# Kernel tuning notes

Hardware: AMD Instinct MI355X
Metric: run time of the kernel (lower is better)

The kernel has to match this reference:

```python
import jax, jax.numpy as jnp
import numpy as np

T, IN_DIM, H1, H2 = 64, 84, 128, 84
BATCH = 8192


def _glorot(key, shape, fan):
    bound = 1.0 / np.sqrt(fan)
    return jax.random.uniform(key, shape, jnp.float32, -bound, bound)


def setup_inputs() -> dict:
    key = jax.random.key(0)
    ks = jax.random.split(key, 13)
    x = jax.random.normal(ks[0], (BATCH, T, IN_DIM, 1), jnp.float32)
    # rnn1 layer 0: 84 -> 128
    w_ih_l0 = _glorot(ks[1], (H1, IN_DIM), H1)
    w_hh_l0 = _glorot(ks[2], (H1, H1), H1)
    b_ih_l0 = _glorot(ks[3], (H1,), H1)
    b_hh_l0 = _glorot(ks[4], (H1,), H1)
    # rnn1 layer 1: 128 -> 128
    w_ih_l1 = _glorot(ks[5], (H1, H1), H1)
    w_hh_l1 = _glorot(ks[6], (H1, H1), H1)
    b_ih_l1 = _glorot(ks[7], (H1,), H1)
    b_hh_l1 = _glorot(ks[8], (H1,), H1)
    # rnn2: 128 -> 84
    w_ih_l2 = _glorot(ks[9], (H2, H1), H2)
    w_hh_l2 = _glorot(ks[10], (H2, H2), H2)
    b_ih_l2 = _glorot(ks[11], (H2,), H2)
    b_hh_l2 = _glorot(ks[12], (H2,), H2)
    return {
        "x": x,
        "w_ih_l0": w_ih_l0, "w_hh_l0": w_hh_l0, "b_ih_l0": b_ih_l0, "b_hh_l0": b_hh_l0,
        "w_ih_l1": w_ih_l1, "w_hh_l1": w_hh_l1, "b_ih_l1": b_ih_l1, "b_hh_l1": b_hh_l1,
        "w_ih_l2": w_ih_l2, "w_hh_l2": w_hh_l2, "b_ih_l2": b_ih_l2, "b_hh_l2": b_hh_l2,
    }


def _elman_layer(x, w_ih, w_hh, b_ih, b_hh):
    # x: (B, T, I) -> (B, T, H); h_t = tanh(x_t W_ih^T + b_ih + h_{t-1} W_hh^T + b_hh)
    # Precompute the input projection for all timesteps as one big GEMM.
    xp = jnp.einsum('bti,hi->bth', x, w_ih) + (b_ih + b_hh)  # (B, T, H)
    h0 = jnp.zeros((x.shape[0], w_hh.shape[0]), x.dtype)

    def step(h, xp_t):
        h = jnp.tanh(xp_t + h @ w_hh.T)
        return h, h

    _, ys = jax.lax.scan(step, h0, jnp.swapaxes(xp, 0, 1))  # (T, B, H)
    return jnp.swapaxes(ys, 0, 1)


def reference(x,
              w_ih_l0, w_hh_l0, b_ih_l0, b_hh_l0,
              w_ih_l1, w_hh_l1, b_ih_l1, b_hh_l1,
              w_ih_l2, w_hh_l2, b_ih_l2, b_hh_l2):
    x_ = jnp.squeeze(x, -1)                                   # (B, 64, 84)
    h = _elman_layer(x_, w_ih_l0, w_hh_l0, b_ih_l0, b_hh_l0)  # (B, 64, 128)
    h = _elman_layer(h, w_ih_l1, w_hh_l1, b_ih_l1, b_hh_l1)   # (B, 64, 128)
    h = _elman_layer(h, w_ih_l2, w_hh_l2, b_ih_l2, b_hh_l2)   # (B, 64, 84)
    return h[..., None]                                       # (B, 64, 84, 1)
```

## Files before the change

kernel.cpp:

```cpp
#include <hip/hip_runtime.h>


typedef __bf16 bf16x8 __attribute__((ext_vector_type(8)));
typedef float  f32x4  __attribute__((ext_vector_type(4)));
typedef float  f32x16 __attribute__((ext_vector_type(16)));
typedef unsigned short u16;
typedef unsigned int   u32;
typedef u16 u16x8 __attribute__((ext_vector_type(8)));
typedef u16 u16x4 __attribute__((ext_vector_type(4)));

#define MFMA32(a, b, c) __builtin_amdgcn_mfma_f32_32x32x16_bf16((a), (b), (c), 0, 0, 0)

__device__ __forceinline__ float bf2f(u16 v) {
    return __builtin_bit_cast(float, (u32)v << 16);
}
__device__ __forceinline__ u16 f2bf(float f) {
    u32 u = __builtin_bit_cast(u32, f);
    u = u + 0x7fffu + ((u >> 16) & 1u);
    return (u16)(u >> 16);
}
__device__ __forceinline__ float tanh_fast(float x) {
    float xc = fminf(fmaxf(x, -12.f), 12.f);
    float e  = __expf(2.f * xc);
    return (e - 1.f) * __builtin_amdgcn_rcpf(e + 1.f);
}
__device__ __forceinline__ bf16x8 ld_lds8(const u16* p) {
    return __builtin_bit_cast(bf16x8, *(const u16x8*)p);
}
__device__ __forceinline__ int aswz(int row, int off) {
    return row * 128 + (off ^ ((row & 7) << 3));
}
__device__ __forceinline__ int xswz(int m, int n) {
    return m * 128 + (n ^ ((m & 7) << 2));
}
__device__ __forceinline__ void store4_hl(u16* ph, u16* pl, f32x4 v) {
    u16x4 hi, lo;
#pragma unroll
    for (int j = 0; j < 4; j++) {
        u16 h = f2bf(v[j]);
        hi[j] = h;
        lo[j] = f2bf(v[j] - bf2f(h));
    }
    *(u16x4*)ph = hi;
    *(u16x4*)pl = lo;
}

struct fragp { bf16x8 h, l; };

__device__ __forceinline__ fragp load_wfrag_hl(const float* W, int Hr, int Kr,
                                               int n, int kbase) {
    u16x8 uh = {0,0,0,0,0,0,0,0}, ul = {0,0,0,0,0,0,0,0};
    if (n < Hr) {
#pragma unroll
        for (int j = 0; j < 8; j++) {
            int k = kbase + j;
            if (k < Kr) {
                float w = W[n * Kr + k];
                u16 hi = f2bf(w);
                uh[j] = hi;
                ul[j] = f2bf(w - bf2f(hi));
            }
        }
    }
    fragp r;
    r.h = __builtin_bit_cast(bf16x8, uh);
    r.l = __builtin_bit_cast(bf16x8, ul);
    return r;
}

__device__ __forceinline__ f32x16 mm3t(const fragp& w, bf16x8 ah, bf16x8 al, f32x16 c) {
    c = MFMA32(w.h, ah, c);
    c = MFMA32(w.l, ah, c);
    c = MFMA32(w.h, al, c);
    return c;
}

__global__ __launch_bounds__(512, 2)
void rnn_fused(const float* __restrict__ x,
               const float* __restrict__ wih0, const float* __restrict__ whh0,
               const float* __restrict__ bih0, const float* __restrict__ bhh0,
               const float* __restrict__ wih1, const float* __restrict__ whh1,
               const float* __restrict__ bih1, const float* __restrict__ bhh1,
               const float* __restrict__ wih2, const float* __restrict__ whh2,
               const float* __restrict__ bih2, const float* __restrict__ bhh2,
               float* __restrict__ out)
{
    __shared__ __align__(16) u16 h0h[2][4096], h0l[2][4096];
    __shared__ __align__(16) u16 h1h[2][4096], h1l[2][4096];
    __shared__ __align__(16) u16 h2h[2][4096], h2l[2][4096];
    __shared__ __align__(16) u16 xbh[2][32][96], xbl[2][32][96];
    __shared__ __align__(16) float xpF[2][4096];
    __shared__ float biasF[3][128];

    const int tid  = threadIdx.x;
    const int wv   = tid >> 6;
    const int lane = tid & 63;
    const int mrow = lane & 31;
    const int q2   = lane >> 5;
    const int kq   = q2 * 8;
    const int q4   = q2 * 4;
    const int aw   = wv & 3;
    const bool isA = (wv < 4);
    const int nb   = aw * 32;
    const int b0   = blockIdx.x * 32;
    const float* xg = x + (long)b0 * 5376;

    { u16* z = &h0h[1][0]; for (int i = tid; i < 4096; i += 512) z[i] = 0; }
    { u16* z = &h0l[1][0]; for (int i = tid; i < 4096; i += 512) z[i] = 0; }
    { u16* z = &h1h[0][0]; for (int i = tid; i < 4096; i += 512) z[i] = 0; }
    { u16* z = &h1l[0][0]; for (int i = tid; i < 4096; i += 512) z[i] = 0; }
    { u16* z = &h2h[1][0]; for (int i = tid; i < 4096; i += 512) z[i] = 0; }
    { u16* z = &h2l[1][0]; for (int i = tid; i < 4096; i += 512) z[i] = 0; }
    for (int i = tid; i < 32 * 12 * 2; i += 512) {
        int par = i / (32 * 12), rem = i - par * 32 * 12;
        int row = rem / 12, col = 84 + rem - row * 12;
        xbh[par][row][col] = 0; xbl[par][row][col] = 0;
    }
    for (int i = tid; i < 32 * 84; i += 512) {
        int row = i / 84, col = i - row * 84;
        float v = xg[(long)row * 5376 + col];
        u16 hi = f2bf(v);
        xbh[0][row][col] = hi;
        xbl[0][row][col] = f2bf(v - bf2f(hi));
    }
    for (int i = tid; i < 384; i += 512) {
        int l = i >> 7, n = i & 127;
        float v = 0.f;
        if (l == 0)      v = bih0[n] + bhh0[n];
        else if (l == 1) v = bih1[n] + bhh1[n];
        else if (n < 84) v = bih2[n] + bhh2[n];
        biasF[l][n] = v;
    }

    __syncthreads();

    if (isA) {
        fragp fhh0[8], fih2[8], fhh2[6];
#pragma unroll
        for (int c = 0; c < 8; c++) {
            fhh0[c] = load_wfrag_hl(whh0, 128, 128, nb + mrow, c * 16 + kq);
            fih2[c] = load_wfrag_hl(wih2,  84, 128, nb + mrow, c * 16 + kq);
        }
#pragma unroll
        for (int c = 0; c < 6; c++)
            fhh2[c] = load_wfrag_hl(whh2, 84, 84, nb + mrow, c * 16 + kq);

        float xs[6];
        for (int rr = 0; rr < 67; ++rr) {
            const int P = rr & 1, PN = P ^ 1;

            if (rr <= 62) {
#pragma unroll
                for (int j = 0; j < 6; j++) {
                    int i = tid + j * 512;
                    if (i < 2688) {
                        int row = i / 84, cc = i - row * 84;
                        xs[j] = xg[(long)row * 5376 + (rr + 1) * 84 + cc];
                    }
                }
            }

            if (rr >= 1 && rr <= 64) {
                f32x16 acc;
#pragma unroll
                for (int g = 0; g < 4; g++) {
                    f32x4 v = *(const f32x4*)&xpF[P][xswz(mrow, nb + g * 8 + q4)];
                    acc[4*g+0] = v[0]; acc[4*g+1] = v[1];
                    acc[4*g+2] = v[2]; acc[4*g+3] = v[3];
                }
                __builtin_amdgcn_s_setprio(1);
#pragma unroll
                for (int c = 0; c < 8; c++) {
                    const int idx = aswz(mrow, c * 16 + kq);
                    acc = mm3t(fhh0[c], ld_lds8(&h0h[P][idx]), ld_lds8(&h0l[P][idx]), acc);
                }
                __builtin_amdgcn_s_setprio(0);
#pragma unroll
                for (int g = 0; g < 4; g++) {
                    const int col = nb + g * 8 + q4;
                    f32x4 v;
                    v[0] = tanh_fast(acc[4*g+0]); v[1] = tanh_fast(acc[4*g+1]);
                    v[2] = tanh_fast(acc[4*g+2]); v[3] = tanh_fast(acc[4*g+3]);
                    const int idx = mrow * 128 + (col ^ ((mrow & 7) << 3));
                    store4_hl(&h0h[PN][idx], &h0l[PN][idx], v);
                }
            }

            if (aw != 3 && rr >= 3) {
                const int t2 = rr - 3;
                f32x16 acc;
#pragma unroll
                for (int g = 0; g < 4; g++) {
                    f32x4 v = *(const f32x4*)&biasF[2][nb + g * 8 + q4];
                    acc[4*g+0] = v[0]; acc[4*g+1] = v[1];
                    acc[4*g+2] = v[2]; acc[4*g+3] = v[3];
                }
                __builtin_amdgcn_s_setprio(1);
#pragma unroll
                for (int c = 0; c < 8; c++) {
                    const int idx = aswz(mrow, c * 16 + kq);
                    acc = mm3t(fih2[c], ld_lds8(&h1h[P][idx]), ld_lds8(&h1l[P][idx]), acc);
                }
#pragma unroll
                for (int c = 0; c < 6; c++) {
                    const int idx = aswz(mrow, c * 16 + kq);
                    acc = mm3t(fhh2[c], ld_lds8(&h2h[P][idx]), ld_lds8(&h2l[P][idx]), acc);
                }
                __builtin_amdgcn_s_setprio(0);
#pragma unroll
                for (int g = 0; g < 4; g++) {
                    const int col = nb + g * 8 + q4;
                    f32x4 v;
                    v[0] = tanh_fast(acc[4*g+0]); v[1] = tanh_fast(acc[4*g+1]);
                    v[2] = tanh_fast(acc[4*g+2]); v[3] = tanh_fast(acc[4*g+3]);
                    const int idx = mrow * 128 + (col ^ ((mrow & 7) << 3));
                    store4_hl(&h2h[PN][idx], &h2l[PN][idx], v);
                    if (col < 84)
                        *(f32x4*)(out + (long)(b0 + mrow) * 5376 + t2 * 84 + col) = v;
                }
            }

            if (rr <= 62) {
#pragma unroll
                for (int j = 0; j < 6; j++) {
                    int i = tid + j * 512;
                    if (i < 2688) {
                        int row = i / 84, cc = i - row * 84;
                        u16 hi = f2bf(xs[j]);
                        xbh[PN][row][cc] = hi;
                        xbl[PN][row][cc] = f2bf(xs[j] - bf2f(hi));
                    }
                }
            }
            __syncthreads();
        }
    } else {
        fragp fih0[6], fih1[8], fhh1[8];
#pragma unroll
        for (int c = 0; c < 6; c++)
            fih0[c] = load_wfrag_hl(wih0, 128, 84, nb + mrow, c * 16 + kq);
#pragma unroll
        for (int c = 0; c < 8; c++) {
            fih1[c] = load_wfrag_hl(wih1, 128, 128, nb + mrow, c * 16 + kq);
            fhh1[c] = load_wfrag_hl(whh1, 128, 128, nb + mrow, c * 16 + kq);
        }

        float xs[6];
        for (int rr = 0; rr < 67; ++rr) {
            const int P = rr & 1, PN = P ^ 1;

            if (rr <= 62) {
#pragma unroll
                for (int j = 0; j < 6; j++) {
                    int i = tid + j * 512;
                    if (i < 2688) {
                        int row = i / 84, cc = i - row * 84;
                        xs[j] = xg[(long)row * 5376 + (rr + 1) * 84 + cc];
                    }
                }
            }

            if (rr >= 2 && rr <= 65) {
                f32x16 acc;
#pragma unroll
                for (int g = 0; g < 4; g++) {
                    f32x4 v = *(const f32x4*)&biasF[1][nb + g * 8 + q4];
                    acc[4*g+0] = v[0]; acc[4*g+1] = v[1];
                    acc[4*g+2] = v[2]; acc[4*g+3] = v[3];
                }
                __builtin_amdgcn_s_setprio(1);
#pragma unroll
                for (int c = 0; c < 8; c++) {
                    const int idx = aswz(mrow, c * 16 + kq);
                    acc = mm3t(fih1[c], ld_lds8(&h0h[P][idx]), ld_lds8(&h0l[P][idx]), acc);
                }
#pragma unroll
                for (int c = 0; c < 8; c++) {
                    const int idx = aswz(mrow, c * 16 + kq);
                    acc = mm3t(fhh1[c], ld_lds8(&h1h[P][idx]), ld_lds8(&h1l[P][idx]), acc);
                }
                __builtin_amdgcn_s_setprio(0);
#pragma unroll
                for (int g = 0; g < 4; g++) {
                    const int col = nb + g * 8 + q4;
                    f32x4 v;
                    v[0] = tanh_fast(acc[4*g+0]); v[1] = tanh_fast(acc[4*g+1]);
                    v[2] = tanh_fast(acc[4*g+2]); v[3] = tanh_fast(acc[4*g+3]);
                    const int idx = mrow * 128 + (col ^ ((mrow & 7) << 3));
                    store4_hl(&h1h[PN][idx], &h1l[PN][idx], v);
                }
            }

            if (rr <= 63) {
                f32x16 acc;
#pragma unroll
                for (int g = 0; g < 4; g++) {
                    f32x4 v = *(const f32x4*)&biasF[0][nb + g * 8 + q4];
                    acc[4*g+0] = v[0]; acc[4*g+1] = v[1];
                    acc[4*g+2] = v[2]; acc[4*g+3] = v[3];
                }
                __builtin_amdgcn_s_setprio(1);
#pragma unroll
                for (int c = 0; c < 6; c++) {
                    const int off = c * 16 + kq;
                    bf16x8 ah = ld_lds8(&xbh[P][mrow][off]);
                    bf16x8 al = ld_lds8(&xbl[P][mrow][off]);
                    acc = mm3t(fih0[c], ah, al, acc);
                }
                __builtin_amdgcn_s_setprio(0);
#pragma unroll
                for (int g = 0; g < 4; g++) {
                    const int n = nb + g * 8 + q4;
                    f32x4 v;
                    v[0] = acc[4*g+0]; v[1] = acc[4*g+1];
                    v[2] = acc[4*g+2]; v[3] = acc[4*g+3];
                    *(f32x4*)&xpF[PN][xswz(mrow, n)] = v;
                }
            }

            if (rr <= 62) {
#pragma unroll
                for (int j = 0; j < 6; j++) {
                    int i = tid + j * 512;
                    if (i < 2688) {
                        int row = i / 84, cc = i - row * 84;
                        u16 hi = f2bf(xs[j]);
                        xbh[PN][row][cc] = hi;
                        xbl[PN][row][cc] = f2bf(xs[j] - bf2f(hi));
                    }
                }
            }
            __syncthreads();
        }
    }
}

extern "C" void kernel_launch(void* const* d_in, const int* in_sizes, int n_in,
                              void* d_out, int out_size, void* d_ws, size_t ws_size,
                              hipStream_t stream) {
    (void)in_sizes; (void)n_in; (void)out_size; (void)d_ws; (void)ws_size;
    const float* x    = (const float*)d_in[0];
    const float* wih0 = (const float*)d_in[1];
    const float* whh0 = (const float*)d_in[2];
    const float* bih0 = (const float*)d_in[3];
    const float* bhh0 = (const float*)d_in[4];
    const float* wih1 = (const float*)d_in[5];
    const float* whh1 = (const float*)d_in[6];
    const float* bih1 = (const float*)d_in[7];
    const float* bhh1 = (const float*)d_in[8];
    const float* wih2 = (const float*)d_in[9];
    const float* whh2 = (const float*)d_in[10];
    const float* bih2 = (const float*)d_in[11];
    const float* bhh2 = (const float*)d_in[12];
    float* out = (float*)d_out;

    rnn_fused<<<dim3(8192 / 32), dim3(512), 0, stream>>>(
        x, wih0, whh0, bih0, bhh0, wih1, whh1, bih1, bhh1,
        wih2, whh2, bih2, bhh2, out);
}
```

Measured before the change: 558.5 us.

## Split fused RNN into per-layer wave groups across 12 waves

```diff
diff --git a/kernel.cpp b/kernel.cpp
--- a/kernel.cpp
+++ b/kernel.cpp
@@ -29,9 +29,6 @@
 }
 __device__ __forceinline__ int aswz(int row, int off) {
     return row * 128 + (off ^ ((row & 7) << 3));
-}
-__device__ __forceinline__ int xswz(int m, int n) {
-    return m * 128 + (n ^ ((m & 7) << 2));
 }
 __device__ __forceinline__ void store4_hl(u16* ph, u16* pl, f32x4 v) {
     u16x4 hi, lo;
@@ -75,7 +72,31 @@
     return c;
 }
 
-__global__ __launch_bounds__(512, 2)
+#define STG_ISSUE(trr)                                                   \
+    {                                                                    \
+        const int tofs = (trr) * 84;                                     \
+        _Pragma("unroll")                                                \
+        for (int j = 0; j < 5; j++) xs[j] = xg[goff[j] + tofs];          \
+        if (tid_s < 128) xs[5] = xg[goff[5] + tofs];                     \
+    }
+#define STG_WRITE(PNv)                                                   \
+    {                                                                    \
+        u16* bh = (&xbh[0][0][0]) + (PNv) * 3072;                        \
+        u16* bl = (&xbl[0][0][0]) + (PNv) * 3072;                        \
+        _Pragma("unroll")                                                \
+        for (int j = 0; j < 5; j++) {                                    \
+            u16 hi = f2bf(xs[j]);                                        \
+            bh[lofs[j]] = hi;                                            \
+            bl[lofs[j]] = f2bf(xs[j] - bf2f(hi));                        \
+        }                                                                \
+        if (tid_s < 128) {                                               \
+            u16 hi = f2bf(xs[5]);                                        \
+            bh[lofs[5]] = hi;                                            \
+            bl[lofs[5]] = f2bf(xs[5] - bf2f(hi));                        \
+        }                                                                \
+    }
+
+__global__ __launch_bounds__(768, 3)
 void rnn_fused(const float* __restrict__ x,
                const float* __restrict__ wih0, const float* __restrict__ whh0,
                const float* __restrict__ bih0, const float* __restrict__ bhh0,
@@ -89,7 +110,6 @@
     __shared__ __align__(16) u16 h1h[2][4096], h1l[2][4096];
     __shared__ __align__(16) u16 h2h[2][4096], h2l[2][4096];
     __shared__ __align__(16) u16 xbh[2][32][96], xbl[2][32][96];
-    __shared__ __align__(16) float xpF[2][4096];
     __shared__ float biasF[3][128];
 
     const int tid  = threadIdx.x;
@@ -99,31 +119,28 @@
     const int q2   = lane >> 5;
     const int kq   = q2 * 8;
     const int q4   = q2 * 4;
-    const int aw   = wv & 3;
-    const bool isA = (wv < 4);
-    const int nb   = aw * 32;
     const int b0   = blockIdx.x * 32;
     const float* xg = x + (long)b0 * 5376;
 
-    { u16* z = &h0h[1][0]; for (int i = tid; i < 4096; i += 512) z[i] = 0; }
-    { u16* z = &h0l[1][0]; for (int i = tid; i < 4096; i += 512) z[i] = 0; }
-    { u16* z = &h1h[0][0]; for (int i = tid; i < 4096; i += 512) z[i] = 0; }
-    { u16* z = &h1l[0][0]; for (int i = tid; i < 4096; i += 512) z[i] = 0; }
-    { u16* z = &h2h[1][0]; for (int i = tid; i < 4096; i += 512) z[i] = 0; }
-    { u16* z = &h2l[1][0]; for (int i = tid; i < 4096; i += 512) z[i] = 0; }
-    for (int i = tid; i < 32 * 12 * 2; i += 512) {
+    { u16* z = &h0h[0][0]; for (int i = tid; i < 4096; i += 768) z[i] = 0; }
+    { u16* z = &h0l[0][0]; for (int i = tid; i < 4096; i += 768) z[i] = 0; }
+    { u16* z = &h1h[1][0]; for (int i = tid; i < 4096; i += 768) z[i] = 0; }
+    { u16* z = &h1l[1][0]; for (int i = tid; i < 4096; i += 768) z[i] = 0; }
+    { u16* z = &h2h[0][0]; for (int i = tid; i < 4096; i += 768) z[i] = 0; }
+    { u16* z = &h2l[0][0]; for (int i = tid; i < 4096; i += 768) z[i] = 0; }
+    for (int i = tid; i < 32 * 12 * 2; i += 768) {
         int par = i / (32 * 12), rem = i - par * 32 * 12;
         int row = rem / 12, col = 84 + rem - row * 12;
         xbh[par][row][col] = 0; xbl[par][row][col] = 0;
     }
-    for (int i = tid; i < 32 * 84; i += 512) {
+    for (int i = tid; i < 2688; i += 768) {
         int row = i / 84, col = i - row * 84;
         float v = xg[(long)row * 5376 + col];
         u16 hi = f2bf(v);
         xbh[0][row][col] = hi;
         xbl[0][row][col] = f2bf(v - bf2f(hi));
     }
-    for (int i = tid; i < 384; i += 512) {
+    for (int i = tid; i < 384; i += 768) {
         int l = i >> 7, n = i & 127;
         float v = 0.f;
         if (l == 0)      v = bih0[n] + bhh0[n];
@@ -131,44 +148,44 @@
         else if (n < 84) v = bih2[n] + bhh2[n];
         biasF[l][n] = v;
     }
-
     __syncthreads();
 
-    if (isA) {
-        fragp fhh0[8], fih2[8], fhh2[6];
-#pragma unroll
-        for (int c = 0; c < 8; c++) {
+    if (wv < 4) {
+        const int nb = wv * 32;
+        fragp fih0[6], fhh0[8];
+#pragma unroll
+        for (int c = 0; c < 6; c++)
+            fih0[c] = load_wfrag_hl(wih0, 128, 84, nb + mrow, c * 16 + kq);
+#pragma unroll
+        for (int c = 0; c < 8; c++)
             fhh0[c] = load_wfrag_hl(whh0, 128, 128, nb + mrow, c * 16 + kq);
-            fih2[c] = load_wfrag_hl(wih2,  84, 128, nb + mrow, c * 16 + kq);
-        }
-#pragma unroll
-        for (int c = 0; c < 6; c++)
-            fhh2[c] = load_wfrag_hl(whh2, 84, 84, nb + mrow, c * 16 + kq);
-
+        const int tid_s = wv * 64 + lane;
+        int goff[6], lofs[6];
+#pragma unroll
+        for (int j = 0; j < 6; j++) {
+            int i = tid_s + j * 512, row = i / 84, cc = i - row * 84;
+            goff[j] = row * 5376 + cc; lofs[j] = row * 96 + cc;
+        }
         float xs[6];
-        for (int rr = 0; rr < 67; ++rr) {
+
+        for (int rr = 0; rr < 66; ++rr) {
             const int P = rr & 1, PN = P ^ 1;
-
-            if (rr <= 62) {
-#pragma unroll
-                for (int j = 0; j < 6; j++) {
-                    int i = tid + j * 512;
-                    if (i < 2688) {
-                        int row = i / 84, cc = i - row * 84;
-                        xs[j] = xg[(long)row * 5376 + (rr + 1) * 84 + cc];
-                    }
-                }
-            }
-
-            if (rr >= 1 && rr <= 64) {
+            if (rr <= 62) STG_ISSUE(rr + 1);
+            if (rr <= 63) {
                 f32x16 acc;
 #pragma unroll
                 for (int g = 0; g < 4; g++) {
-                    f32x4 v = *(const f32x4*)&xpF[P][xswz(mrow, nb + g * 8 + q4)];
+                    f32x4 v = *(const f32x4*)&biasF[0][nb + g * 8 + q4];
                     acc[4*g+0] = v[0]; acc[4*g+1] = v[1];
                     acc[4*g+2] = v[2]; acc[4*g+3] = v[3];
                 }
                 __builtin_amdgcn_s_setprio(1);
+#pragma unroll
+                for (int c = 0; c < 6; c++) {
+                    const int off = c * 16 + kq;
+                    acc = mm3t(fih0[c], ld_lds8(&xbh[P][mrow][off]),
+                                        ld_lds8(&xbl[P][mrow][off]), acc);
+                }
 #pragma unroll
                 for (int c = 0; c < 8; c++) {
                     const int idx = aswz(mrow, c * 16 + kq);
@@ -185,9 +202,74 @@
                     store4_hl(&h0h[PN][idx], &h0l[PN][idx], v);
                 }
             }
-
-            if (aw != 3 && rr >= 3) {
-                const int t2 = rr - 3;
+            if (rr <= 62) STG_WRITE(PN);
+            __syncthreads();
+        }
+    } else if (wv < 8) {
+        const int nb = (wv - 4) * 32;
+        fragp fih1[8], fhh1[8];
+#pragma unroll
+        for (int c = 0; c < 8; c++) {
+            fih1[c] = load_wfrag_hl(wih1, 128, 128, nb + mrow, c * 16 + kq);
+            fhh1[c] = load_wfrag_hl(whh1, 128, 128, nb + mrow, c * 16 + kq);
+        }
+        for (int rr = 0; rr < 66; ++rr) {
+            const int P = rr & 1, PN = P ^ 1;
+            if (rr >= 1 && rr <= 64) {
+                f32x16 acc;
+#pragma unroll
+                for (int g = 0; g < 4; g++) {
+                    f32x4 v = *(const f32x4*)&biasF[1][nb + g * 8 + q4];
+                    acc[4*g+0] = v[0]; acc[4*g+1] = v[1];
+                    acc[4*g+2] = v[2]; acc[4*g+3] = v[3];
+                }
+                __builtin_amdgcn_s_setprio(1);
+#pragma unroll
+                for (int c = 0; c < 8; c++) {
+                    const int idx = aswz(mrow, c * 16 + kq);
+                    acc = mm3t(fih1[c], ld_lds8(&h0h[P][idx]), ld_lds8(&h0l[P][idx]), acc);
+                }
+#pragma unroll
+                for (int c = 0; c < 8; c++) {
+                    const int idx = aswz(mrow, c * 16 + kq);
+                    acc = mm3t(fhh1[c], ld_lds8(&h1h[P][idx]), ld_lds8(&h1l[P][idx]), acc);
+                }
+                __builtin_amdgcn_s_setprio(0);
+#pragma unroll
+                for (int g = 0; g < 4; g++) {
+                    const int col = nb + g * 8 + q4;
+                    f32x4 v;
+                    v[0] = tanh_fast(acc[4*g+0]); v[1] = tanh_fast(acc[4*g+1]);
+                    v[2] = tanh_fast(acc[4*g+2]); v[3] = tanh_fast(acc[4*g+3]);
+                    const int idx = mrow * 128 + (col ^ ((mrow & 7) << 3));
+                    store4_hl(&h1h[PN][idx], &h1l[PN][idx], v);
+                }
+            }
+            __syncthreads();
+        }
+    } else if (wv < 11) {
+        const int nb = (wv - 8) * 32;
+        fragp fih2[8], fhh2[6];
+#pragma unroll
+        for (int c = 0; c < 8; c++)
+            fih2[c] = load_wfrag_hl(wih2, 84, 128, nb + mrow, c * 16 + kq);
+#pragma unroll
+        for (int c = 0; c < 6; c++)
+            fhh2[c] = load_wfrag_hl(whh2, 84, 84, nb + mrow, c * 16 + kq);
+        const int tid_s = (wv - 4) * 64 + lane;
+        int goff[6], lofs[6];
+#pragma unroll
+        for (int j = 0; j < 6; j++) {
+            int i = tid_s + j * 512, row = i / 84, cc = i - row * 84;
+            goff[j] = row * 5376 + cc; lofs[j] = row * 96 + cc;
+        }
+        float xs[6];
+
+        for (int rr = 0; rr < 66; ++rr) {
+            const int P = rr & 1, PN = P ^ 1;
+            if (rr <= 62) STG_ISSUE(rr + 1);
+            if (rr >= 2) {
+                const int t2 = rr - 2;
                 f32x16 acc;
 #pragma unroll
                 for (int g = 0; g < 4; g++) {
@@ -219,117 +301,22 @@
                         *(f32x4*)(out + (long)(b0 + mrow) * 5376 + t2 * 84 + col) = v;
                 }
             }
-
-            if (rr <= 62) {
-#pragma unroll
-                for (int j = 0; j < 6; j++) {
-                    int i = tid + j * 512;
-                    if (i < 2688) {
-                        int row = i / 84, cc = i - row * 84;
-                        u16 hi = f2bf(xs[j]);
-                        xbh[PN][row][cc] = hi;
-                        xbl[PN][row][cc] = f2bf(xs[j] - bf2f(hi));
-                    }
-                }
-            }
+            if (rr <= 62) STG_WRITE(PN);
             __syncthreads();
         }
     } else {
-        fragp fih0[6], fih1[8], fhh1[8];
-#pragma unroll
-        for (int c = 0; c < 6; c++)
-            fih0[c] = load_wfrag_hl(wih0, 128, 84, nb + mrow, c * 16 + kq);
-#pragma unroll
-        for (int c = 0; c < 8; c++) {
-            fih1[c] = load_wfrag_hl(wih1, 128, 128, nb + mrow, c * 16 + kq);
-            fhh1[c] = load_wfrag_hl(whh1, 128, 128, nb + mrow, c * 16 + kq);
-        }
-
+        const int tid_s = 7 * 64 + lane;
+        int goff[6], lofs[6];
+#pragma unroll
+        for (int j = 0; j < 6; j++) {
+            int i = tid_s + j * 512, row = i / 84, cc = i - row * 84;
+            goff[j] = row * 5376 + cc; lofs[j] = row * 96 + cc;
+        }
         float xs[6];
-        for (int rr = 0; rr < 67; ++rr) {
-            const int P = rr & 1, PN = P ^ 1;
-
-            if (rr <= 62) {
-#pragma unroll
-                for (int j = 0; j < 6; j++) {
-                    int i = tid + j * 512;
-                    if (i < 2688) {
-                        int row = i / 84, cc = i - row * 84;
-                        xs[j] = xg[(long)row * 5376 + (rr + 1) * 84 + cc];
-                    }
-                }
-            }
-
-            if (rr >= 2 && rr <= 65) {
-                f32x16 acc;
-#pragma unroll
-                for (int g = 0; g < 4; g++) {
-                    f32x4 v = *(const f32x4*)&biasF[1][nb + g * 8 + q4];
-                    acc[4*g+0] = v[0]; acc[4*g+1] = v[1];
-                    acc[4*g+2] = v[2]; acc[4*g+3] = v[3];
-                }
-                __builtin_amdgcn_s_setprio(1);
-#pragma unroll
-                for (int c = 0; c < 8; c++) {
-                    const int idx = aswz(mrow, c * 16 + kq);
-                    acc = mm3t(fih1[c], ld_lds8(&h0h[P][idx]), ld_lds8(&h0l[P][idx]), acc);
-                }
-#pragma unroll
-                for (int c = 0; c < 8; c++) {
-                    const int idx = aswz(mrow, c * 16 + kq);
-                    acc = mm3t(fhh1[c], ld_lds8(&h1h[P][idx]), ld_lds8(&h1l[P][idx]), acc);
-                }
-                __builtin_amdgcn_s_setprio(0);
-#pragma unroll
-                for (int g = 0; g < 4; g++) {
-                    const int col = nb + g * 8 + q4;
-                    f32x4 v;
-                    v[0] = tanh_fast(acc[4*g+0]); v[1] = tanh_fast(acc[4*g+1]);
-                    v[2] = tanh_fast(acc[4*g+2]); v[3] = tanh_fast(acc[4*g+3]);
-                    const int idx = mrow * 128 + (col ^ ((mrow & 7) << 3));
-                    store4_hl(&h1h[PN][idx], &h1l[PN][idx], v);
-                }
-            }
-
-            if (rr <= 63) {
-                f32x16 acc;
-#pragma unroll
-                for (int g = 0; g < 4; g++) {
-                    f32x4 v = *(const f32x4*)&biasF[0][nb + g * 8 + q4];
-                    acc[4*g+0] = v[0]; acc[4*g+1] = v[1];
-                    acc[4*g+2] = v[2]; acc[4*g+3] = v[3];
-                }
-                __builtin_amdgcn_s_setprio(1);
-#pragma unroll
-                for (int c = 0; c < 6; c++) {
-                    const int off = c * 16 + kq;
-                    bf16x8 ah = ld_lds8(&xbh[P][mrow][off]);
-                    bf16x8 al = ld_lds8(&xbl[P][mrow][off]);
-                    acc = mm3t(fih0[c], ah, al, acc);
-                }
-                __builtin_amdgcn_s_setprio(0);
-#pragma unroll
-                for (int g = 0; g < 4; g++) {
-                    const int n = nb + g * 8 + q4;
-                    f32x4 v;
-                    v[0] = acc[4*g+0]; v[1] = acc[4*g+1];
-                    v[2] = acc[4*g+2]; v[3] = acc[4*g+3];
-                    *(f32x4*)&xpF[PN][xswz(mrow, n)] = v;
-                }
-            }
-
-            if (rr <= 62) {
-#pragma unroll
-                for (int j = 0; j < 6; j++) {
-                    int i = tid + j * 512;
-                    if (i < 2688) {
-                        int row = i / 84, cc = i - row * 84;
-                        u16 hi = f2bf(xs[j]);
-                        xbh[PN][row][cc] = hi;
-                        xbl[PN][row][cc] = f2bf(xs[j] - bf2f(hi));
-                    }
-                }
-            }
+        for (int rr = 0; rr < 66; ++rr) {
+            const int PN = (rr & 1) ^ 1;
+            if (rr <= 62) STG_ISSUE(rr + 1);
+            if (rr <= 62) STG_WRITE(PN);
             __syncthreads();
         }
     }
@@ -354,7 +341,7 @@
     const float* bhh2 = (const float*)d_in[12];
     float* out = (float*)d_out;
 
-    rnn_fused<<<dim3(8192 / 32), dim3(512), 0, stream>>>(
+    rnn_fused<<<dim3(8192 / 32), dim3(768), 0, stream>>>(
         x, wih0, whh0, bih0, bhh0, wih1, whh1, bih1, bhh1,
         wih2, whh2, bih2, bhh2, out);
 }
```

Measured after the change: 555.5 us. No clear change (-0.5%).
